# Kernel optimization log

Hardware: AMD Instinct MI355X
Metric: run time of the kernel (lower is better)

Reference implementation:

```python
import jax, jax.numpy as jnp
import numpy as np

B, T, S, D, K = 512, 49, 200, 512, 128


def setup_inputs() -> dict:
    key = jax.random.key(0)
    ks = jax.random.split(key, 8)
    return {
        "ifeature": jax.random.normal(ks[0], (B, T, D), dtype=jnp.float32),
        "tfeature_h": jax.random.normal(ks[1], (B, S, D), dtype=jnp.float32),
        "w_Dense_Vi_0": jax.random.normal(ks[2], (D, K), dtype=jnp.float32) * 0.05,
        "w_Dense_Vt_0": jax.random.normal(ks[3], (D, K), dtype=jnp.float32) * 0.05,
        "w_Dense_Pi_0": jax.random.normal(ks[4], (2 * K, 1), dtype=jnp.float32) * 0.05,
        "b_Dense_Pi_0": jnp.zeros((T,), dtype=jnp.float32),
        "w_Dense_Vi_1": jax.random.normal(ks[5], (D, K), dtype=jnp.float32) * 0.05,
        "w_Dense_Vt_1": jax.random.normal(ks[6], (D, K), dtype=jnp.float32) * 0.05,
        "w_Dense_Pi_1": jax.random.normal(ks[7], (2 * K, 1), dtype=jnp.float32) * 0.05,
        "b_Dense_Pi_1": jnp.zeros((S,), dtype=jnp.float32),
    }


def reference(ifeature, tfeature_h, w_Dense_Vi_0, w_Dense_Vt_0, w_Dense_Pi_0,
              b_Dense_Pi_0, w_Dense_Vi_1, w_Dense_Vt_1, w_Dense_Pi_1, b_Dense_Pi_1):
    # tfeature: mean-pooled text, [B, D]
    tfeature = jnp.mean(tfeature_h, axis=1)

    # --- attention over image regions (title_len) ---
    w_Vi_0 = jnp.einsum('btd,dk->btk', ifeature, w_Dense_Vi_0)          # [B,T,K]
    w_Vt_0 = (tfeature @ w_Dense_Vt_0)[:, None, :]                      # [B,1,K] broadcast to T
    Hi = jnp.tanh(jnp.concatenate(
        [w_Vi_0, jnp.broadcast_to(w_Vt_0, w_Vi_0.shape)], axis=-1))     # [B,T,2K]
    Hi_w_b = jnp.einsum('btk,k->bt', Hi, w_Dense_Pi_0[:, 0]) + b_Dense_Pi_0
    Pi = jax.nn.softmax(Hi_w_b, axis=-1)                                # [B,T]
    Vi = jnp.einsum('bt,btd->bd', Pi, ifeature)                         # attended image feature

    # --- attention over text tokens (seq_len) ---
    w_Vi_1 = (Vi @ w_Dense_Vi_1)[:, None, :]                            # [B,1,K]
    w_Vt_1 = jnp.einsum('bsd,dk->bsk', tfeature_h, w_Dense_Vt_1)        # [B,S,K]
    Ht = jnp.tanh(jnp.concatenate(
        [jnp.broadcast_to(w_Vi_1, w_Vt_1.shape), w_Vt_1], axis=-1))     # [B,S,2K]
    Ht_b = jnp.einsum('bsk,k->bs', Ht, w_Dense_Pi_1[:, 0]) + b_Dense_Pi_1
    Pt = jax.nn.softmax(Ht_b, axis=-1)                                  # [B,S]

    # NOTE: original call() returns Pt_Vt (weighted tokens), not the pooled Vt.
    Pt_Vt = Pt[:, :, None] * tfeature_h                                 # [B,S,D]
    return Pt_Vt
```

## Files before the change

kernel.cpp:

```cpp
#include <hip/hip_runtime.h>
#include <math.h>

#define BB 512
#define SS 200
#define DD 512
#define KK 128
#define RR (BB * SS)

typedef __attribute__((ext_vector_type(8))) short bf16x8;
typedef __attribute__((ext_vector_type(4))) float f32x4;

__device__ inline unsigned short f2bf(float f) {
    union { float f; unsigned int u; } v; v.f = f;
    unsigned int r = v.u + 0x7FFFu + ((v.u >> 16) & 1u);
    return (unsigned short)(r >> 16);
}

__global__ void wt_kernel(const float* __restrict__ W, unsigned short* __restrict__ Wt) {
    int i = blockIdx.x * 256 + threadIdx.x;
    int col = i >> 9, d = i & 511;
    Wt[i] = f2bf(W[d * KK + col]);
}

__global__ __launch_bounds__(256, 2) void logits_mfma_kernel(
    const float* __restrict__ A,
    const unsigned short* __restrict__ Wt,
    const float* __restrict__ wpk,
    const float* __restrict__ bias,
    float* __restrict__ out)
{
    __shared__ unsigned short As[128][40];
    __shared__ unsigned short Bs[128][40];

    int tid = threadIdx.x;
    int w = tid >> 6;
    int l = tid & 63;
    int l15 = l & 15;
    int g = l >> 4;
    size_t row0 = (size_t)blockIdx.x * 128;

    f32x4 acc[2][8];
    #pragma unroll
    for (int m = 0; m < 2; ++m)
        #pragma unroll
        for (int n = 0; n < 8; ++n) acc[m][n] = (f32x4){0.f, 0.f, 0.f, 0.f};

    float wv[8];
    #pragma unroll
    for (int n = 0; n < 8; ++n) wv[n] = wpk[n * 16 + l15];

    int ar = tid >> 1;
    int ac = (tid & 1) * 16;
    int bc = tid >> 1;
    int bh = (tid & 1) * 16;

    for (int d0 = 0; d0 < DD; d0 += 32) {
        {
            const float* src = A + (row0 + ar) * DD + d0 + ac;
            float4 v0 = *(const float4*)(src);
            float4 v1 = *(const float4*)(src + 4);
            float4 v2 = *(const float4*)(src + 8);
            float4 v3 = *(const float4*)(src + 12);
            bf16x8 p0, p1;
            p0[0] = (short)f2bf(v0.x); p0[1] = (short)f2bf(v0.y);
            p0[2] = (short)f2bf(v0.z); p0[3] = (short)f2bf(v0.w);
            p0[4] = (short)f2bf(v1.x); p0[5] = (short)f2bf(v1.y);
            p0[6] = (short)f2bf(v1.z); p0[7] = (short)f2bf(v1.w);
            p1[0] = (short)f2bf(v2.x); p1[1] = (short)f2bf(v2.y);
            p1[2] = (short)f2bf(v2.z); p1[3] = (short)f2bf(v2.w);
            p1[4] = (short)f2bf(v3.x); p1[5] = (short)f2bf(v3.y);
            p1[6] = (short)f2bf(v3.z); p1[7] = (short)f2bf(v3.w);
            *(bf16x8*)&As[ar][ac]     = p0;
            *(bf16x8*)&As[ar][ac + 8] = p1;
        }
        {
            const unsigned short* src = Wt + (size_t)bc * DD + d0 + bh;
            bf16x8 q0 = *(const bf16x8*)(src);
            bf16x8 q1 = *(const bf16x8*)(src + 8);
            *(bf16x8*)&Bs[bc][bh]     = q0;
            *(bf16x8*)&Bs[bc][bh + 8] = q1;
        }
        __syncthreads();
        bf16x8 afrag[2];
        #pragma unroll
        for (int m = 0; m < 2; ++m)
            afrag[m] = *(const bf16x8*)&As[w * 32 + m * 16 + l15][g * 8];
        #pragma unroll
        for (int n = 0; n < 8; ++n) {
            bf16x8 bfrag = *(const bf16x8*)&Bs[n * 16 + l15][g * 8];
            acc[0][n] = __builtin_amdgcn_mfma_f32_16x16x32_bf16(afrag[0], bfrag, acc[0][n], 0, 0, 0);
            acc[1][n] = __builtin_amdgcn_mfma_f32_16x16x32_bf16(afrag[1], bfrag, acc[1][n], 0, 0, 0);
        }
        __syncthreads();
    }

    float rs[2][4];
    #pragma unroll
    for (int m = 0; m < 2; ++m)
        #pragma unroll
        for (int r = 0; r < 4; ++r) rs[m][r] = 0.f;
    #pragma unroll
    for (int m = 0; m < 2; ++m)
        #pragma unroll
        for (int n = 0; n < 8; ++n)
            #pragma unroll
            for (int r = 0; r < 4; ++r)
                rs[m][r] += tanhf(acc[m][n][r]) * wv[n];

    #pragma unroll
    for (int m = 0; m < 2; ++m)
        #pragma unroll
        for (int r = 0; r < 4; ++r) {
            float v = rs[m][r];
            v += __shfl_xor(v, 1, 64);
            v += __shfl_xor(v, 2, 64);
            v += __shfl_xor(v, 4, 64);
            v += __shfl_xor(v, 8, 64);
            rs[m][r] = v;
        }
    if (l15 == 0) {
        #pragma unroll
        for (int m = 0; m < 2; ++m)
            #pragma unroll
            for (int r = 0; r < 4; ++r) {
                int grow = (int)row0 + w * 32 + m * 16 + g * 4 + r;
                out[grow] = rs[m][r] + bias[grow % SS];
            }
    }
}

__global__ __launch_bounds__(1024) void softmax_mul_kernel(
    const float* __restrict__ logits,
    const float* __restrict__ tfh,
    float* __restrict__ out)
{
    int b = blockIdx.x;
    int tid = threadIdx.x;
    __shared__ float Pt[SS];
    __shared__ float wpart[16];

    float v = (tid < SS) ? logits[(size_t)b * SS + tid] : -INFINITY;
    float m = v;
    #pragma unroll
    for (int off = 32; off > 0; off >>= 1) m = fmaxf(m, __shfl_xor(m, off, 64));
    if ((tid & 63) == 0) wpart[tid >> 6] = m;
    __syncthreads();
    m = -INFINITY;
    #pragma unroll
    for (int i = 0; i < 16; ++i) m = fmaxf(m, wpart[i]);
    float e = (tid < SS) ? expf(v - m) : 0.f;
    float ssum = e;
    #pragma unroll
    for (int off = 32; off > 0; off >>= 1) ssum += __shfl_xor(ssum, off, 64);
    __syncthreads();
    if ((tid & 63) == 0) wpart[tid >> 6] = ssum;
    __syncthreads();
    ssum = 0.f;
    #pragma unroll
    for (int i = 0; i < 16; ++i) ssum += wpart[i];
    if (tid < SS) Pt[tid] = e / ssum;
    __syncthreads();

    const float4* src = (const float4*)(tfh + (size_t)b * SS * DD);
    float4*       dst = (float4*)(out + (size_t)b * SS * DD);
    const int n4 = SS * DD / 4;
    for (int i = tid; i < n4; i += 1024) {
        float p = Pt[i >> 7];
        float4 x = src[i];
        x.x *= p; x.y *= p; x.z *= p; x.w *= p;
        dst[i] = x;
    }
}

extern "C" void kernel_launch(void* const* d_in, const int* in_sizes, int n_in,
                              void* d_out, int out_size, void* d_ws, size_t ws_size,
                              hipStream_t stream) {
    const float* tfh   = (const float*)d_in[1];
    const float* wVt1  = (const float*)d_in[7];
    const float* wp1   = (const float*)d_in[8];
    const float* bias1 = (const float*)d_in[9];
    float* out = (float*)d_out;

    unsigned short* Wt = (unsigned short*)d_ws;
    float* logits = (float*)((char*)d_ws + KK * DD * sizeof(unsigned short));

    wt_kernel<<<KK * DD / 256, 256, 0, stream>>>(wVt1, Wt);
    logits_mfma_kernel<<<RR / 128, 256, 0, stream>>>(tfh, Wt, wp1 + KK, bias1, logits);
    softmax_mul_kernel<<<BB, 1024, 0, stream>>>(logits, tfh, out);
}
```

Measured before the change: 141.0 us.

## Double-buffer LDS tiles and prefetch next K-slice in logits MFMA kernel

Converts the logits GEMM main loop to a register-prefetch, double-buffered LDS pipeline. The next 32-wide slice of A and Wt is loaded into registers before the MFMAs on the current buffer and written to the other buffer afterward, so one barrier per iteration replaces two. This is meant to hide global load latency behind MFMA work. The launch bound occupancy hint rises from 2 to 3 blocks per CU, which doubles LDS use and may raise register pressure from the held prefetch values.

```diff
diff --git a/kernel.cpp b/kernel.cpp
--- a/kernel.cpp
+++ b/kernel.cpp
@@ -22,21 +22,20 @@
     Wt[i] = f2bf(W[d * KK + col]);
 }
 
-__global__ __launch_bounds__(256, 2) void logits_mfma_kernel(
+__global__ __launch_bounds__(256, 3) void logits_mfma_kernel(
     const float* __restrict__ A,
     const unsigned short* __restrict__ Wt,
     const float* __restrict__ wpk,
     const float* __restrict__ bias,
     float* __restrict__ out)
 {
-    __shared__ unsigned short As[128][40];
-    __shared__ unsigned short Bs[128][40];
+    __shared__ unsigned short As[2][128][40];
+    __shared__ unsigned short Bs[2][128][40];
 
     int tid = threadIdx.x;
     int w = tid >> 6;
-    int l = tid & 63;
-    int l15 = l & 15;
-    int g = l >> 4;
+    int l15 = tid & 15;
+    int g = (tid & 63) >> 4;
     size_t row0 = (size_t)blockIdx.x * 128;
 
     f32x4 acc[2][8];
@@ -51,46 +50,55 @@
 
     int ar = tid >> 1;
     int ac = (tid & 1) * 16;
-    int bc = tid >> 1;
-    int bh = (tid & 1) * 16;
+    const float*          aptr = A  + (row0 + ar) * DD + ac;
+    const unsigned short* bptr = Wt + (size_t)ar * DD + ac;
 
-    for (int d0 = 0; d0 < DD; d0 += 32) {
-        {
-            const float* src = A + (row0 + ar) * DD + d0 + ac;
-            float4 v0 = *(const float4*)(src);
-            float4 v1 = *(const float4*)(src + 4);
-            float4 v2 = *(const float4*)(src + 8);
-            float4 v3 = *(const float4*)(src + 12);
-            bf16x8 p0, p1;
-            p0[0] = (short)f2bf(v0.x); p0[1] = (short)f2bf(v0.y);
-            p0[2] = (short)f2bf(v0.z); p0[3] = (short)f2bf(v0.w);
-            p0[4] = (short)f2bf(v1.x); p0[5] = (short)f2bf(v1.y);
-            p0[6] = (short)f2bf(v1.z); p0[7] = (short)f2bf(v1.w);
-            p1[0] = (short)f2bf(v2.x); p1[1] = (short)f2bf(v2.y);
-            p1[2] = (short)f2bf(v2.z); p1[3] = (short)f2bf(v2.w);
-            p1[4] = (short)f2bf(v3.x); p1[5] = (short)f2bf(v3.y);
-            p1[6] = (short)f2bf(v3.z); p1[7] = (short)f2bf(v3.w);
-            *(bf16x8*)&As[ar][ac]     = p0;
-            *(bf16x8*)&As[ar][ac + 8] = p1;
-        }
-        {
-            const unsigned short* src = Wt + (size_t)bc * DD + d0 + bh;
-            bf16x8 q0 = *(const bf16x8*)(src);
-            bf16x8 q1 = *(const bf16x8*)(src + 8);
-            *(bf16x8*)&Bs[bc][bh]     = q0;
-            *(bf16x8*)&Bs[bc][bh + 8] = q1;
-        }
-        __syncthreads();
-        bf16x8 afrag[2];
-        #pragma unroll
-        for (int m = 0; m < 2; ++m)
-            afrag[m] = *(const bf16x8*)&As[w * 32 + m * 16 + l15][g * 8];
+    float4 sa0, sa1, sa2, sa3;
+    bf16x8 sb0, sb1;
+
+    #define LOADT(d0) do {                                   \
+        const float* s_ = aptr + (d0);                       \
+        sa0 = *(const float4*)(s_);                          \
+        sa1 = *(const float4*)(s_ + 4);                      \
+        sa2 = *(const float4*)(s_ + 8);                      \
+        sa3 = *(const float4*)(s_ + 12);                     \
+        const unsigned short* t_ = bptr + (d0);              \
+        sb0 = *(const bf16x8*)(t_);                          \
+        sb1 = *(const bf16x8*)(t_ + 8);                      \
+    } while (0)
+
+    #define WRITET(buf) do {                                 \
+        bf16x8 p0_, p1_;                                     \
+        p0_[0] = (short)f2bf(sa0.x); p0_[1] = (short)f2bf(sa0.y); \
+        p0_[2] = (short)f2bf(sa0.z); p0_[3] = (short)f2bf(sa0.w); \
+        p0_[4] = (short)f2bf(sa1.x); p0_[5] = (short)f2bf(sa1.y); \
+        p0_[6] = (short)f2bf(sa1.z); p0_[7] = (short)f2bf(sa1.w); \
+        p1_[0] = (short)f2bf(sa2.x); p1_[1] = (short)f2bf(sa2.y); \
+        p1_[2] = (short)f2bf(sa2.z); p1_[3] = (short)f2bf(sa2.w); \
+        p1_[4] = (short)f2bf(sa3.x); p1_[5] = (short)f2bf(sa3.y); \
+        p1_[6] = (short)f2bf(sa3.z); p1_[7] = (short)f2bf(sa3.w); \
+        *(bf16x8*)&As[buf][ar][ac]     = p0_;                \
+        *(bf16x8*)&As[buf][ar][ac + 8] = p1_;                \
+        *(bf16x8*)&Bs[buf][ar][ac]     = sb0;                \
+        *(bf16x8*)&Bs[buf][ar][ac + 8] = sb1;                \
+    } while (0)
+
+    LOADT(0);
+    WRITET(0);
+    __syncthreads();
+
+    for (int t = 0; t < 16; ++t) {
+        int p = t & 1;
+        if (t < 15) LOADT((t + 1) * 32);
+        bf16x8 af0 = *(const bf16x8*)&As[p][w * 32 + l15][g * 8];
+        bf16x8 af1 = *(const bf16x8*)&As[p][w * 32 + 16 + l15][g * 8];
         #pragma unroll
         for (int n = 0; n < 8; ++n) {
-            bf16x8 bfrag = *(const bf16x8*)&Bs[n * 16 + l15][g * 8];
-            acc[0][n] = __builtin_amdgcn_mfma_f32_16x16x32_bf16(afrag[0], bfrag, acc[0][n], 0, 0, 0);
-            acc[1][n] = __builtin_amdgcn_mfma_f32_16x16x32_bf16(afrag[1], bfrag, acc[1][n], 0, 0, 0);
+            bf16x8 bf = *(const bf16x8*)&Bs[p][n * 16 + l15][g * 8];
+            acc[0][n] = __builtin_amdgcn_mfma_f32_16x16x32_bf16(af0, bf, acc[0][n], 0, 0, 0);
+            acc[1][n] = __builtin_amdgcn_mfma_f32_16x16x32_bf16(af1, bf, acc[1][n], 0, 0, 0);
         }
+        if (t < 15) WRITET(p ^ 1);
         __syncthreads();
     }
 
```

Measured after the change: 146.9 us. 1.04x slower.

## Fuse logits GEMM with softmax and weighting into one per-batch kernel

Applied to the files above, without the earlier changes.

Merges the MFMA logits kernel and the softmax/multiply kernel into a single kernel with one 512-thread block per batch row. Logits stay in shared memory, and the second read of the batch's token features may come from cache since the same block just loaded them. In exchange, each block pads 200 rows to 256, doing extra GEMM work, and the grid shrinks to one block per batch, which lowers parallelism.

```diff
diff --git a/kernel.cpp b/kernel.cpp
--- a/kernel.cpp
+++ b/kernel.cpp
@@ -5,7 +5,6 @@
 #define SS 200
 #define DD 512
 #define KK 128
-#define RR (BB * SS)
 
 typedef __attribute__((ext_vector_type(8))) short bf16x8;
 typedef __attribute__((ext_vector_type(4))) float f32x4;
@@ -22,22 +21,26 @@
     Wt[i] = f2bf(W[d * KK + col]);
 }
 
-__global__ __launch_bounds__(256, 2) void logits_mfma_kernel(
-    const float* __restrict__ A,
+__global__ __launch_bounds__(512, 4) void fused_kernel(
+    const float* __restrict__ tfh,
     const unsigned short* __restrict__ Wt,
     const float* __restrict__ wpk,
     const float* __restrict__ bias,
     float* __restrict__ out)
 {
-    __shared__ unsigned short As[128][40];
+    __shared__ unsigned short As[256][40];
     __shared__ unsigned short Bs[128][40];
+    __shared__ float logit_s[256];
+    __shared__ float Pt[SS];
+    __shared__ float wpart[8];
 
     int tid = threadIdx.x;
-    int w = tid >> 6;
-    int l = tid & 63;
+    int w   = tid >> 6;
+    int l   = tid & 63;
     int l15 = l & 15;
-    int g = l >> 4;
-    size_t row0 = (size_t)blockIdx.x * 128;
+    int g   = l >> 4;
+    int b   = blockIdx.x;
+    const float* Ab = tfh + (size_t)b * SS * DD;
 
     f32x4 acc[2][8];
     #pragma unroll
@@ -49,18 +52,19 @@
     #pragma unroll
     for (int n = 0; n < 8; ++n) wv[n] = wpk[n * 16 + l15];
 
-    int ar = tid >> 1;
-    int ac = (tid & 1) * 16;
-    int bc = tid >> 1;
-    int bh = (tid & 1) * 16;
+    int ar  = tid >> 1;
+    int arc = (ar < SS) ? ar : (SS - 1);
+    int ac  = (tid & 1) * 16;
+    const float* aptr = Ab + (size_t)arc * DD + ac;
+    const unsigned short* bptr = Wt + (size_t)(tid >> 1) * DD + ac;
 
     for (int d0 = 0; d0 < DD; d0 += 32) {
         {
-            const float* src = A + (row0 + ar) * DD + d0 + ac;
-            float4 v0 = *(const float4*)(src);
-            float4 v1 = *(const float4*)(src + 4);
-            float4 v2 = *(const float4*)(src + 8);
-            float4 v3 = *(const float4*)(src + 12);
+            const float* s_ = aptr + d0;
+            float4 v0 = *(const float4*)(s_);
+            float4 v1 = *(const float4*)(s_ + 4);
+            float4 v2 = *(const float4*)(s_ + 8);
+            float4 v3 = *(const float4*)(s_ + 12);
             bf16x8 p0, p1;
             p0[0] = (short)f2bf(v0.x); p0[1] = (short)f2bf(v0.y);
             p0[2] = (short)f2bf(v0.z); p0[3] = (short)f2bf(v0.w);
@@ -73,23 +77,20 @@
             *(bf16x8*)&As[ar][ac]     = p0;
             *(bf16x8*)&As[ar][ac + 8] = p1;
         }
-        {
-            const unsigned short* src = Wt + (size_t)bc * DD + d0 + bh;
-            bf16x8 q0 = *(const bf16x8*)(src);
-            bf16x8 q1 = *(const bf16x8*)(src + 8);
-            *(bf16x8*)&Bs[bc][bh]     = q0;
-            *(bf16x8*)&Bs[bc][bh + 8] = q1;
+        if (tid < 256) {
+            bf16x8 q0 = *(const bf16x8*)(bptr + d0);
+            bf16x8 q1 = *(const bf16x8*)(bptr + d0 + 8);
+            *(bf16x8*)&Bs[tid >> 1][ac]     = q0;
+            *(bf16x8*)&Bs[tid >> 1][ac + 8] = q1;
         }
         __syncthreads();
-        bf16x8 afrag[2];
-        #pragma unroll
-        for (int m = 0; m < 2; ++m)
-            afrag[m] = *(const bf16x8*)&As[w * 32 + m * 16 + l15][g * 8];
+        bf16x8 af0 = *(const bf16x8*)&As[w * 32 + l15][g * 8];
+        bf16x8 af1 = *(const bf16x8*)&As[w * 32 + 16 + l15][g * 8];
         #pragma unroll
         for (int n = 0; n < 8; ++n) {
-            bf16x8 bfrag = *(const bf16x8*)&Bs[n * 16 + l15][g * 8];
-            acc[0][n] = __builtin_amdgcn_mfma_f32_16x16x32_bf16(afrag[0], bfrag, acc[0][n], 0, 0, 0);
-            acc[1][n] = __builtin_amdgcn_mfma_f32_16x16x32_bf16(afrag[1], bfrag, acc[1][n], 0, 0, 0);
+            bf16x8 bf = *(const bf16x8*)&Bs[n * 16 + l15][g * 8];
+            acc[0][n] = __builtin_amdgcn_mfma_f32_16x16x32_bf16(af0, bf, acc[0][n], 0, 0, 0);
+            acc[1][n] = __builtin_amdgcn_mfma_f32_16x16x32_bf16(af1, bf, acc[1][n], 0, 0, 0);
         }
         __syncthreads();
     }
@@ -106,7 +107,6 @@
             #pragma unroll
             for (int r = 0; r < 4; ++r)
                 rs[m][r] += tanhf(acc[m][n][r]) * wv[n];
-
     #pragma unroll
     for (int m = 0; m < 2; ++m)
         #pragma unroll
@@ -123,48 +123,38 @@
         for (int m = 0; m < 2; ++m)
             #pragma unroll
             for (int r = 0; r < 4; ++r) {
-                int grow = (int)row0 + w * 32 + m * 16 + g * 4 + r;
-                out[grow] = rs[m][r] + bias[grow % SS];
+                int srow = w * 32 + m * 16 + g * 4 + r;
+                if (srow < SS) logit_s[srow] = rs[m][r] + bias[srow];
             }
     }
-}
+    __syncthreads();
 
-__global__ __launch_bounds__(1024) void softmax_mul_kernel(
-    const float* __restrict__ logits,
-    const float* __restrict__ tfh,
-    float* __restrict__ out)
-{
-    int b = blockIdx.x;
-    int tid = threadIdx.x;
-    __shared__ float Pt[SS];
-    __shared__ float wpart[16];
-
-    float v = (tid < SS) ? logits[(size_t)b * SS + tid] : -INFINITY;
+    float v = (tid < SS) ? logit_s[tid] : -INFINITY;
     float m = v;
     #pragma unroll
     for (int off = 32; off > 0; off >>= 1) m = fmaxf(m, __shfl_xor(m, off, 64));
-    if ((tid & 63) == 0) wpart[tid >> 6] = m;
+    if (l == 0) wpart[w] = m;
     __syncthreads();
     m = -INFINITY;
     #pragma unroll
-    for (int i = 0; i < 16; ++i) m = fmaxf(m, wpart[i]);
+    for (int i = 0; i < 8; ++i) m = fmaxf(m, wpart[i]);
     float e = (tid < SS) ? expf(v - m) : 0.f;
     float ssum = e;
     #pragma unroll
     for (int off = 32; off > 0; off >>= 1) ssum += __shfl_xor(ssum, off, 64);
     __syncthreads();
-    if ((tid & 63) == 0) wpart[tid >> 6] = ssum;
+    if (l == 0) wpart[w] = ssum;
     __syncthreads();
     ssum = 0.f;
     #pragma unroll
-    for (int i = 0; i < 16; ++i) ssum += wpart[i];
+    for (int i = 0; i < 8; ++i) ssum += wpart[i];
     if (tid < SS) Pt[tid] = e / ssum;
     __syncthreads();
 
-    const float4* src = (const float4*)(tfh + (size_t)b * SS * DD);
+    const float4* src = (const float4*)Ab;
     float4*       dst = (float4*)(out + (size_t)b * SS * DD);
     const int n4 = SS * DD / 4;
-    for (int i = tid; i < n4; i += 1024) {
+    for (int i = tid; i < n4; i += 512) {
         float p = Pt[i >> 7];
         float4 x = src[i];
         x.x *= p; x.y *= p; x.z *= p; x.w *= p;
@@ -182,9 +172,7 @@
     float* out = (float*)d_out;
 
     unsigned short* Wt = (unsigned short*)d_ws;
-    float* logits = (float*)((char*)d_ws + KK * DD * sizeof(unsigned short));
 
     wt_kernel<<<KK * DD / 256, 256, 0, stream>>>(wVt1, Wt);
-    logits_mfma_kernel<<<RR / 128, 256, 0, stream>>>(tfh, Wt, wp1 + KK, bias1, logits);
-    softmax_mul_kernel<<<BB, 1024, 0, stream>>>(logits, tfh, out);
+    fused_kernel<<<BB, 512, 0, stream>>>(tfh, Wt, wp1 + KK, bias1, out);
 }
```

Result: faster. 135.3 us (-4.0%).
